# Performance work log

Hardware: AMD Instinct MI355X
Metric: run time of the kernel (lower is better)

## Reference

```python
import jax, jax.numpy as jnp
import numpy as np

N_NODES = 100000
N_EDGES = 1600000
F_IN = 512    # args.in_channels (original node feature dim)
F_GNN = 128   # GCNConv output / 'in_channels' ctor arg
HID = 64
Z_DIM = 64
N_GRAPHS = 512


def setup_inputs() -> dict:
    key = jax.random.key(0)
    ks = jax.random.split(key, 20)
    x = jax.random.normal(ks[0], (N_NODES, F_IN), dtype=jnp.float32)
    edge_index = jax.random.randint(ks[1], (2, N_EDGES), 0, N_NODES)
    batch = jnp.sort(jax.random.randint(ks[2], (N_NODES,), 0, N_GRAPHS))
    eps = jax.random.normal(ks[3], (N_GRAPHS, Z_DIM), dtype=jnp.float32)

    def lin(k, fi, fo):
        # xavier_uniform weight, zero bias
        lim = float(np.sqrt(6.0 / (fi + fo)))
        W = jax.random.uniform(k, (fi, fo), minval=-lim, maxval=lim, dtype=jnp.float32)
        return W, jnp.zeros((fo,), dtype=jnp.float32)

    Wg, bg = lin(ks[4], F_IN, F_GNN)
    We1, be1 = lin(ks[5], 2 * F_GNN, HID)
    We2, be2 = lin(ks[6], HID, HID)
    We3, be3 = lin(ks[7], HID, 2 * Z_DIM)
    Wd1, bd1 = lin(ks[8], Z_DIM, HID)
    Wd2, bd2 = lin(ks[9], HID, HID)
    Wd3, bd3 = lin(ks[10], HID, F_GNN)
    return {"x": x, "edge_index": edge_index, "batch": batch, "eps": eps,
            "Wg": Wg, "bg": bg,
            "We1": We1, "be1": be1, "We2": We2, "be2": be2, "We3": We3, "be3": be3,
            "Wd1": Wd1, "bd1": bd1, "Wd2": Wd2, "bd2": bd2, "Wd3": Wd3, "bd3": bd3}


def _gcn_conv(x, edge_index, Wg, bg):
    # PyG GCNConv: add self-loops, symmetric deg normalization, linear-then-aggregate
    n = x.shape[0]
    loops = jnp.arange(n)
    src = jnp.concatenate([edge_index[0], loops])
    dst = jnp.concatenate([edge_index[1], loops])
    deg = jax.ops.segment_sum(jnp.ones_like(dst, dtype=x.dtype), dst, num_segments=n)
    dinv = jnp.where(deg > 0, jax.lax.rsqrt(jnp.maximum(deg, 1.0)), 0.0)
    norm = dinv[src] * dinv[dst]              # [E+N]
    xw = x @ Wg                               # [N, F_GNN]
    msg = xw[src] * norm[:, None]             # gather + scale: [E+N, F_GNN]
    agg = jax.ops.segment_sum(msg, dst, num_segments=n)
    return agg + bg


def _forward(x, edge_index, batch, eps,
             Wg, bg, We1, be1, We2, be2, We3, be3,
             Wd1, bd1, Wd2, bd2, Wd3, bd3):
    n = x.shape[0]
    g = eps.shape[0]
    # single GNN layer (num_layers=1, JK='last'); dropout omitted (eval determinism)
    node_x = jax.nn.relu(_gcn_conv(x, edge_index, Wg, bg))  # [N, F_GNN]
    # global mean / max pool by graph id
    ones = jnp.ones((n,), dtype=node_x.dtype)
    cnt = jax.ops.segment_sum(ones, batch, num_segments=g)
    mean_p = jax.ops.segment_sum(node_x, batch, num_segments=g) / jnp.maximum(cnt, 1.0)[:, None]
    max_p = jax.ops.segment_max(node_x, batch, num_segments=g)
    graph_x = jnp.concatenate([mean_p, max_p], axis=1)      # [G, 2*F_GNN]
    # gaussian encoder MLP
    t = jax.nn.elu(graph_x @ We1 + be1)
    t = jnp.tanh(t @ We2 + be2)
    ml = t @ We3 + be3
    mu, logvar = jnp.split(ml, 2, axis=1)
    # reparameterise (note: module returns stddev in the 'logvar' slot)
    stddev = 1e-6 + jax.nn.softplus(logvar)
    z = mu + eps * stddev
    # bernoulli decoder MLP
    d = jnp.tanh(z @ Wd1 + bd1)
    d = jax.nn.elu(d @ Wd2 + bd2)
    y = jax.nn.sigmoid(d @ Wd3 + bd3)
    y = jnp.clip(y, 1e-8, 1.0 - 1e-8)
    return mu, stddev, y


def reference(x, edge_index, batch, eps,
              Wg, bg, We1, be1, We2, be2, We3, be3,
              Wd1, bd1, Wd2, bd2, Wd3, bd3):
    return _forward(x, edge_index, batch, eps,
                    Wg, bg, We1, be1, We2, be2, We3, be3,
                    Wd1, bd1, Wd2, bd2, Wd3, bd3)
```

## Files before the change

### kernel.cpp

```cpp
#include <hip/hip_runtime.h>
#include <hip/hip_bf16.h>
#include <math.h>

#define N_NODES 100000
#define N_EDGES 1600000
#define F_IN 512
#define F_GNN 128
#define HID 64
#define Z_DIM 64
#define N_GRAPHS 512
#define N_REGIONS 196
#define REGION_CAP 10240

typedef __attribute__((ext_vector_type(8))) short short8;
typedef __attribute__((ext_vector_type(4))) float f32x4;

__device__ __forceinline__ float eluf(float v) { return v > 0.f ? v : expm1f(v); }
__device__ __forceinline__ float softplusf(float v) {
  return fmaxf(v, 0.f) + log1pf(expf(-fabsf(v)));
}
__device__ __forceinline__ float sigmoidf(float v) { return 1.f / (1.f + expf(-v)); }

__device__ __forceinline__ unsigned short f2bf(float f) {
  unsigned int u = __float_as_uint(f);
  u = (u + 0x7fffu + ((u >> 16) & 1u)) >> 16;
  return (unsigned short)u;
}
__device__ __forceinline__ unsigned int f2bf2(float a, float b) {
  __hip_bfloat162 h = __float22bfloat162_rn(make_float2(a, b));
  unsigned int u;
  __builtin_memcpy(&u, &h, 4);
  return u;
}
__device__ __forceinline__ float bf_lo(unsigned int u) { return __uint_as_float(u << 16); }
__device__ __forceinline__ float bf_hi(unsigned int u) { return __uint_as_float(u & 0xffff0000u); }

__device__ __forceinline__ int lower_bound_i(const int* __restrict__ a, int n, int v) {
  int lo = 0, hi = n;
  while (lo < hi) {
    int mid = (lo + hi) >> 1;
    if (a[mid] < v) lo = mid + 1; else hi = mid;
  }
  return lo;
}

__global__ void k_wg(const float* __restrict__ Wg, unsigned short* __restrict__ WgT,
                     int* __restrict__ rcnt) {
  int i = blockIdx.x * 256 + threadIdx.x;
  if (blockIdx.x == 0) rcnt[threadIdx.x] = 0;
  int n = i >> 9, k = i & 511;
  WgT[i] = f2bf(Wg[k * F_GNN + n]);
}

__global__ __launch_bounds__(256) void k_rcount(const int* __restrict__ ei,
                                                int* __restrict__ rcnt) {
  __shared__ int lh[256];
  const int b = blockIdx.x, t = threadIdx.x;
  lh[t] = 0;
  __syncthreads();
#pragma unroll
  for (int j = 0; j < 8; j++) {
    int e = b * 2048 + t + 256 * j;
    if (e < N_EDGES) atomicAdd(&lh[ei[N_EDGES + e] >> 9], 1);
  }
  __syncthreads();
  if (t < N_REGIONS && lh[t] > 0) atomicAdd(&rcnt[t], lh[t]);
}

__global__ __launch_bounds__(256) void k_rscan(int* __restrict__ rcnt,
                                               int* __restrict__ rbase) {
  __shared__ int s[256];
  int t = threadIdx.x;
  s[t] = (t < N_REGIONS) ? rcnt[t] : 0;
  __syncthreads();
#pragma unroll
  for (int d = 1; d < 256; d <<= 1) {
    int v = (t >= d) ? s[t - d] : 0;
    __syncthreads();
    s[t] += v;
    __syncthreads();
  }
  int excl = (t > 0) ? s[t - 1] : 0;
  rbase[t] = excl;
  rcnt[t] = excl;
  if (t == 255) rbase[N_REGIONS] = s[255];
}

__global__ __launch_bounds__(256) void k_bucket(
    const int* __restrict__ ei, int* __restrict__ cursor_r,
    uint2* __restrict__ pairs) {
  __shared__ int lhist[256];
  __shared__ int lofs[256];
  __shared__ int lcur[256];
  __shared__ int gbase[256];
  __shared__ int sc[256];
  __shared__ uint2 lpairs[4096];

  const int b = blockIdx.x, t = threadIdx.x;
  const int e0 = b * 4096;
  const int n_b = min(4096, N_EDGES - e0);

  lhist[t] = 0;
  lcur[t] = 0;
  __syncthreads();

  int srcv[16], dstv[16];
#pragma unroll
  for (int j = 0; j < 16; j++) {
    int e = e0 + t + 256 * j;
    if (e < N_EDGES) {
      srcv[j] = ei[e];
      dstv[j] = ei[N_EDGES + e];
      atomicAdd(&lhist[dstv[j] >> 9], 1);
    } else {
      dstv[j] = -1;
    }
  }
  __syncthreads();

  sc[t] = lhist[t];
  __syncthreads();
#pragma unroll
  for (int d = 1; d < 256; d <<= 1) {
    int v = (t >= d) ? sc[t - d] : 0;
    __syncthreads();
    sc[t] += v;
    __syncthreads();
  }
  lofs[t] = (t > 0) ? sc[t - 1] : 0;
  if (t < N_REGIONS && lhist[t] > 0) gbase[t] = atomicAdd(&cursor_r[t], lhist[t]);
  __syncthreads();

#pragma unroll
  for (int j = 0; j < 16; j++) {
    if (dstv[j] >= 0) {
      int r = dstv[j] >> 9;
      int pos = lofs[r] + atomicAdd(&lcur[r], 1);
      lpairs[pos] = make_uint2((unsigned)srcv[j], (unsigned)dstv[j]);
    }
  }
  __syncthreads();

  for (int i = t; i < n_b; i += 256) {
    int lo = 0, hi = N_REGIONS;
    while (hi - lo > 1) {
      int mid = (lo + hi) >> 1;
      if (lofs[mid] <= i) lo = mid; else hi = mid;
    }
    pairs[gbase[lo] + (i - lofs[lo])] = lpairs[i];
  }
}

__global__ __launch_bounds__(256) void k_region(
    const uint2* __restrict__ pairs, const int* __restrict__ rbase,
    int* __restrict__ off, float* __restrict__ dinv, int* __restrict__ csr_src) {
  __shared__ int nh[512];
  __shared__ int sofs[512];
  __shared__ int sc[256];
  __shared__ int ncur[512];
  __shared__ int cbuf[REGION_CAP];

  const int r = blockIdx.x, t = threadIdx.x;
  const int base = rbase[r];
  const int cnt = rbase[r + 1] - base;

  nh[t] = 0;
  nh[t + 256] = 0;
  __syncthreads();

  for (int i = t; i < cnt; i += 256) {
    uint2 p = pairs[base + i];
    atomicAdd(&nh[p.y & 511], 1);
  }
  __syncthreads();

  int a0 = nh[2 * t], a1 = nh[2 * t + 1];
  sc[t] = a0 + a1;
  __syncthreads();
#pragma unroll
  for (int d = 1; d < 256; d <<= 1) {
    int v = (t >= d) ? sc[t - d] : 0;
    __syncthreads();
    sc[t] += v;
    __syncthreads();
  }
  int excl = (t > 0) ? sc[t - 1] : 0;
  sofs[2 * t] = excl;
  sofs[2 * t + 1] = excl + a0;

  const int node0 = r << 9;
  int n0 = node0 + 2 * t;
  if (n0 < N_NODES)     { off[n0] = base + excl;      dinv[n0] = rsqrtf(1.f + (float)a0); }
  if (n0 + 1 < N_NODES) { off[n0 + 1] = base + excl + a0; dinv[n0 + 1] = rsqrtf(1.f + (float)a1); }
  if (r == N_REGIONS - 1 && t == 0) off[N_NODES] = N_EDGES;

  ncur[t] = 0;
  ncur[t + 256] = 0;
  __syncthreads();

  for (int i = t; i < cnt; i += 256) {
    uint2 p = pairs[base + i];
    int d = (int)p.y & 511;
    int lpos = sofs[d] + atomicAdd(&ncur[d], 1);
    if (lpos < REGION_CAP) cbuf[lpos] = (int)p.x;
  }
  __syncthreads();
  for (int i = t; i < cnt; i += 256) csr_src[base + i] = cbuf[i];
}

__global__ __launch_bounds__(256) void k_gemm(
    const float* __restrict__ x, const unsigned short* __restrict__ WgT,
    const float* __restrict__ dinv, unsigned short* __restrict__ sxw) {
  __shared__ unsigned short As[128][32];
  __shared__ unsigned short Bs[128][32];

  const int t = threadIdx.x;
  const int lane15 = t & 15;
  const int quad = (t & 63) >> 4;
  const int wave = t >> 6;
  const int wm = (wave & 1) * 64;
  const int wn = (wave >> 1) * 64;
  const int row0 = blockIdx.x * 128;

  f32x4 acc[4][4];
#pragma unroll
  for (int mi = 0; mi < 4; mi++)
#pragma unroll
    for (int ni = 0; ni < 4; ni++) acc[mi][ni] = (f32x4){0.f, 0.f, 0.f, 0.f};

  float4 ga[4];
  uint4 gb[2];
  auto load_tile = [&](int k0) {
#pragma unroll
    for (int i = 0; i < 4; i++) {
      int f = t + 256 * i;
      int r = f >> 3, c4 = f & 7;
      int gr = row0 + r;
      if (gr >= N_NODES) gr = N_NODES - 1;
      ga[i] = *(const float4*)&x[(size_t)gr * F_IN + k0 + c4 * 4];
    }
#pragma unroll
    for (int i = 0; i < 2; i++) {
      int f = t + 256 * i;
      int r = f >> 2, c = f & 3;
      gb[i] = *(const uint4*)&WgT[r * F_IN + k0 + c * 8];
    }
  };

  load_tile(0);
#pragma unroll 1
  for (int kt = 0; kt < 16; kt++) {
    __syncthreads();
#pragma unroll
    for (int i = 0; i < 4; i++) {
      int f = t + 256 * i;
      int r = f >> 3, c4 = f & 7;
      unsigned int u0 = f2bf2(ga[i].x, ga[i].y);
      unsigned int u1 = f2bf2(ga[i].z, ga[i].w);
      *(uint2*)&As[r][c4 * 4] = make_uint2(u0, u1);
    }
#pragma unroll
    for (int i = 0; i < 2; i++) {
      int f = t + 256 * i;
      int r = f >> 2, c = f & 3;
      *(uint4*)&Bs[r][c * 8] = gb[i];
    }
    __syncthreads();
    if (kt < 15) load_tile((kt + 1) * 32);

    short8 afr[4], bfr[4];
#pragma unroll
    for (int mi = 0; mi < 4; mi++)
      afr[mi] = *(const short8*)&As[wm + mi * 16 + lane15][quad * 8];
#pragma unroll
    for (int ni = 0; ni < 4; ni++)
      bfr[ni] = *(const short8*)&Bs[wn + ni * 16 + lane15][quad * 8];
#pragma unroll
    for (int mi = 0; mi < 4; mi++)
#pragma unroll
      for (int ni = 0; ni < 4; ni++)
        acc[mi][ni] = __builtin_amdgcn_mfma_f32_16x16x32_bf16(
            bfr[ni], afr[mi], acc[mi][ni], 0, 0, 0);
  }

#pragma unroll
  for (int mi = 0; mi < 4; mi++) {
    int gm = row0 + wm + mi * 16 + lane15;
    if (gm < N_NODES) {
      float s = dinv[gm];
#pragma unroll
      for (int ni = 0; ni < 4; ni++) {
        int gn = wn + ni * 16 + quad * 4;
        unsigned int u0 = f2bf2(acc[mi][ni][0] * s, acc[mi][ni][1] * s);
        unsigned int u1 = f2bf2(acc[mi][ni][2] * s, acc[mi][ni][3] * s);
        *(uint2*)&sxw[(size_t)gm * F_GNN + gn] = make_uint2(u0, u1);
      }
    }
  }
}

__global__ __launch_bounds__(1024) void k_aggpool(
    const unsigned short* __restrict__ sxw, const int* __restrict__ off,
    const int* __restrict__ csr_src, const float* __restrict__ dinv,
    const float* __restrict__ bg, const int* __restrict__ batch,
    float* __restrict__ gx) {
  __shared__ float2 ssum[16][64];
  __shared__ float2 smax[16][64];
  __shared__ int sse[2];
  const int g = blockIdx.x;
  const int t = threadIdx.x;
  const int wv = t >> 6;
  const int lane = t & 63;

  if (t == 0) sse[0] = lower_bound_i(batch, N_NODES, g);
  if (t == 64) sse[1] = lower_bound_i(batch, N_NODES, g + 1);
  __syncthreads();
  const int start = sse[0], end = sse[1];

  const unsigned int* S = (const unsigned int*)sxw;
  float2 b = ((const float2*)bg)[lane];
  float2 ps = make_float2(0.f, 0.f);
  float2 pm = make_float2(0.f, 0.f);

  for (int node = start + wv; node < end; node += 16) {
    unsigned int u = S[(size_t)node * 64 + lane];
    float sx = bf_lo(u), sy = bf_hi(u);
    int e = off[node];
    int e1 = off[node + 1];
    for (; e + 7 < e1; e += 8) {
      int s0 = csr_src[e + 0], s1 = csr_src[e + 1];
      int s2 = csr_src[e + 2], s3 = csr_src[e + 3];
      int s4 = csr_src[e + 4], s5 = csr_src[e + 5];
      int s6 = csr_src[e + 6], s7 = csr_src[e + 7];
      unsigned int v0 = S[(size_t)s0 * 64 + lane];
      unsigned int v1 = S[(size_t)s1 * 64 + lane];
      unsigned int v2 = S[(size_t)s2 * 64 + lane];
      unsigned int v3 = S[(size_t)s3 * 64 + lane];
      unsigned int v4 = S[(size_t)s4 * 64 + lane];
      unsigned int v5 = S[(size_t)s5 * 64 + lane];
      unsigned int v6 = S[(size_t)s6 * 64 + lane];
      unsigned int v7 = S[(size_t)s7 * 64 + lane];
      sx += bf_lo(v0) + bf_lo(v1) + bf_lo(v2) + bf_lo(v3)
          + bf_lo(v4) + bf_lo(v5) + bf_lo(v6) + bf_lo(v7);
      sy += bf_hi(v0) + bf_hi(v1) + bf_hi(v2) + bf_hi(v3)
          + bf_hi(v4) + bf_hi(v5) + bf_hi(v6) + bf_hi(v7);
    }
    for (; e < e1; e++) {
      unsigned int v0 = S[(size_t)csr_src[e] * 64 + lane];
      sx += bf_lo(v0);
      sy += bf_hi(v0);
    }
    float di = dinv[node];
    float rx = fmaxf(fmaf(sx, di, b.x), 0.f);
    float ry = fmaxf(fmaf(sy, di, b.y), 0.f);
    ps.x += rx; ps.y += ry;
    pm.x = fmaxf(pm.x, rx); pm.y = fmaxf(pm.y, ry);
  }

  ssum[wv][lane] = ps;
  smax[wv][lane] = pm;
  __syncthreads();
  if (t < 64) {
    float2 s = ssum[0][t];
    float2 m = smax[0][t];
#pragma unroll
    for (int h = 1; h < 16; h++) {
      s.x += ssum[h][t].x; s.y += ssum[h][t].y;
      m.x = fmaxf(m.x, smax[h][t].x); m.y = fmaxf(m.y, smax[h][t].y);
    }
    float ic = 1.f / fmaxf((float)(end - start), 1.f);
    gx[g * 256 + 2 * t] = s.x * ic;
    gx[g * 256 + 2 * t + 1] = s.y * ic;
    gx[g * 256 + 128 + 2 * t] = m.x;
    gx[g * 256 + 129 + 2 * t] = m.y;
  }
}

__global__ __launch_bounds__(64) void k_mlp(
    const float* __restrict__ gx, const float* __restrict__ eps,
    const float* __restrict__ We1, const float* __restrict__ be1,
    const float* __restrict__ We2, const float* __restrict__ be2,
    const float* __restrict__ We3, const float* __restrict__ be3,
    const float* __restrict__ Wd1, const float* __restrict__ bd1,
    const float* __restrict__ Wd2, const float* __restrict__ bd2,
    const float* __restrict__ Wd3, const float* __restrict__ bd3,
    float* __restrict__ out) {
  __shared__ float row[256];
  __shared__ float t1[64], t2[64], zz[64], d1[64], d2[64];
  int g = blockIdx.x;
  int j = threadIdx.x;

#pragma unroll
  for (int i = 0; i < 4; i++) row[j + 64 * i] = gx[g * 256 + j + 64 * i];
  __syncthreads();

  float s = be1[j];
#pragma unroll 4
  for (int k = 0; k < 256; k++) s = fmaf(row[k], We1[k * 64 + j], s);
  t1[j] = eluf(s);
  __syncthreads();

  s = be2[j];
#pragma unroll 4
  for (int k = 0; k < 64; k++) s = fmaf(t1[k], We2[k * 64 + j], s);
  t2[j] = tanhf(s);
  __syncthreads();

  float m = be3[j], lv = be3[64 + j];
#pragma unroll 4
  for (int k = 0; k < 64; k++) {
    float tv = t2[k];
    m = fmaf(tv, We3[k * 128 + j], m);
    lv = fmaf(tv, We3[k * 128 + 64 + j], lv);
  }
  float sd = 1e-6f + softplusf(lv);
  float z = fmaf(eps[g * 64 + j], sd, m);
  out[g * 64 + j] = m;
  out[32768 + g * 64 + j] = sd;
  zz[j] = z;
  __syncthreads();

  s = bd1[j];
#pragma unroll 4
  for (int k = 0; k < 64; k++) s = fmaf(zz[k], Wd1[k * 64 + j], s);
  d1[j] = tanhf(s);
  __syncthreads();

  s = bd2[j];
#pragma unroll 4
  for (int k = 0; k < 64; k++) s = fmaf(d1[k], Wd2[k * 64 + j], s);
  d2[j] = eluf(s);
  __syncthreads();

  float y0 = bd3[j], y1 = bd3[64 + j];
#pragma unroll 4
  for (int k = 0; k < 64; k++) {
    float dv = d2[k];
    y0 = fmaf(dv, Wd3[k * 128 + j], y0);
    y1 = fmaf(dv, Wd3[k * 128 + 64 + j], y1);
  }
  y0 = fminf(fmaxf(sigmoidf(y0), 1e-8f), 1.f - 1e-8f);
  y1 = fminf(fmaxf(sigmoidf(y1), 1e-8f), 1.f - 1e-8f);
  out[65536 + g * 128 + j] = y0;
  out[65536 + g * 128 + 64 + j] = y1;
}

extern "C" void kernel_launch(void* const* d_in, const int* in_sizes, int n_in,
                              void* d_out, int out_size, void* d_ws, size_t ws_size,
                              hipStream_t stream) {
  const float* x     = (const float*)d_in[0];
  const int*   ei    = (const int*)d_in[1];
  const int*   batch = (const int*)d_in[2];
  const float* eps   = (const float*)d_in[3];
  const float* Wg    = (const float*)d_in[4];
  const float* bg    = (const float*)d_in[5];
  const float* We1   = (const float*)d_in[6];
  const float* be1   = (const float*)d_in[7];
  const float* We2   = (const float*)d_in[8];
  const float* be2   = (const float*)d_in[9];
  const float* We3   = (const float*)d_in[10];
  const float* be3   = (const float*)d_in[11];
  const float* Wd1   = (const float*)d_in[12];
  const float* bd1   = (const float*)d_in[13];
  const float* Wd2   = (const float*)d_in[14];
  const float* bd2   = (const float*)d_in[15];
  const float* Wd3   = (const float*)d_in[16];
  const float* bd3   = (const float*)d_in[17];
  float* out = (float*)d_out;

  int*            rbase    = (int*)d_ws;
  int*            cursor_r = rbase + 256;
  int*            off      = cursor_r + 256;
  float*          dinv     = (float*)(off + 102656);
  int*            csr_src  = (int*)(dinv + 102400);
  uint2*          pairs    = (uint2*)(csr_src + 1600128);
  unsigned short* WgT      = (unsigned short*)(pairs + 1600000);
  unsigned short* sxw      = WgT + 65536;
  float*          gx       = (float*)(sxw + 12800000);

  k_wg<<<(F_IN * F_GNN) / 256, 256, 0, stream>>>(Wg, WgT, cursor_r);
  k_rcount<<<(N_EDGES + 2047) / 2048, 256, 0, stream>>>(ei, cursor_r);
  k_rscan<<<1, 256, 0, stream>>>(cursor_r, rbase);
  k_bucket<<<(N_EDGES + 4095) / 4096, 256, 0, stream>>>(ei, cursor_r, pairs);
  k_region<<<N_REGIONS, 256, 0, stream>>>(pairs, rbase, off, dinv, csr_src);
  k_gemm<<<(N_NODES + 127) / 128, 256, 0, stream>>>(x, WgT, dinv, sxw);
  k_aggpool<<<N_GRAPHS, 1024, 0, stream>>>(sxw, off, csr_src, dinv, bg, batch, gx);
  k_mlp<<<N_GRAPHS, 64, 0, stream>>>(gx, eps, We1, be1, We2, be2, We3, be3,
                                     Wd1, bd1, Wd2, bd2, Wd3, bd3, out);
}
```

Measured before the change: 559.4 us.

## Replace CSR build with region-bucketed shared-memory atomic aggregation and atomic pooling

```diff
diff --git a/kernel.cpp b/kernel.cpp
--- a/kernel.cpp
+++ b/kernel.cpp
@@ -10,7 +10,7 @@
 #define Z_DIM 64
 #define N_GRAPHS 512
 #define N_REGIONS 196
-#define REGION_CAP 10240
+#define QTR 128
 
 typedef __attribute__((ext_vector_type(8))) short short8;
 typedef __attribute__((ext_vector_type(4))) float f32x4;
@@ -35,36 +35,46 @@
 __device__ __forceinline__ float bf_lo(unsigned int u) { return __uint_as_float(u << 16); }
 __device__ __forceinline__ float bf_hi(unsigned int u) { return __uint_as_float(u & 0xffff0000u); }
 
-__device__ __forceinline__ int lower_bound_i(const int* __restrict__ a, int n, int v) {
-  int lo = 0, hi = n;
-  while (lo < hi) {
-    int mid = (lo + hi) >> 1;
-    if (a[mid] < v) lo = mid + 1; else hi = mid;
-  }
-  return lo;
-}
-
-__global__ void k_wg(const float* __restrict__ Wg, unsigned short* __restrict__ WgT,
-                     int* __restrict__ rcnt) {
+__global__ __launch_bounds__(256) void k_init(
+    const float* __restrict__ Wg, unsigned short* __restrict__ WgT,
+    int* __restrict__ hist, float* __restrict__ gx, float* __restrict__ gcnt) {
   int i = blockIdx.x * 256 + threadIdx.x;
-  if (blockIdx.x == 0) rcnt[threadIdx.x] = 0;
-  int n = i >> 9, k = i & 511;
-  WgT[i] = f2bf(Wg[k * F_GNN + n]);
-}
-
-__global__ __launch_bounds__(256) void k_rcount(const int* __restrict__ ei,
-                                                int* __restrict__ rcnt) {
-  __shared__ int lh[256];
-  const int b = blockIdx.x, t = threadIdx.x;
-  lh[t] = 0;
-  __syncthreads();
-#pragma unroll
-  for (int j = 0; j < 8; j++) {
-    int e = b * 2048 + t + 256 * j;
-    if (e < N_EDGES) atomicAdd(&lh[ei[N_EDGES + e] >> 9], 1);
-  }
-  __syncthreads();
-  if (t < N_REGIONS && lh[t] > 0) atomicAdd(&rcnt[t], lh[t]);
+  if (i < 65536) {
+    int n = i >> 9, k = i & 511;
+    WgT[i] = f2bf(Wg[k * F_GNN + n]);
+  }
+  if (i < 100352) hist[i] = 0;
+  gx[i] = 0.f;
+  if (i < 512) gcnt[i] = 0.f;
+}
+
+__global__ __launch_bounds__(256) void k_hist(const int* __restrict__ ei,
+                                              int* __restrict__ hist) {
+  int b = blockIdx.x, t = threadIdx.x;
+#pragma unroll
+  for (int j = 0; j < 4; j++) {
+    int e = b * 1024 + t + 256 * j;
+    if (e < N_EDGES) atomicAdd(&hist[ei[N_EDGES + e]], 1);
+  }
+}
+
+__global__ __launch_bounds__(256) void k_rsum(const int* __restrict__ hist,
+                                              float* __restrict__ dinv,
+                                              int* __restrict__ rcnt) {
+  __shared__ int s[256];
+  int r = blockIdx.x, t = threadIdx.x;
+  int n0 = (r << 9) + 2 * t;
+  int a0 = hist[n0], a1 = hist[n0 + 1];
+  if (n0 < N_NODES)     dinv[n0]     = rsqrtf(1.f + (float)a0);
+  if (n0 + 1 < N_NODES) dinv[n0 + 1] = rsqrtf(1.f + (float)a1);
+  s[t] = a0 + a1;
+  __syncthreads();
+#pragma unroll
+  for (int d = 128; d > 0; d >>= 1) {
+    if (t < d) s[t] += s[t + d];
+    __syncthreads();
+  }
+  if (t == 0) rcnt[r] = s[0];
 }
 
 __global__ __launch_bounds__(256) void k_rscan(int* __restrict__ rcnt,
@@ -88,13 +98,13 @@
 
 __global__ __launch_bounds__(256) void k_bucket(
     const int* __restrict__ ei, int* __restrict__ cursor_r,
-    uint2* __restrict__ pairs) {
+    unsigned int* __restrict__ pairs) {
   __shared__ int lhist[256];
   __shared__ int lofs[256];
   __shared__ int lcur[256];
   __shared__ int gbase[256];
   __shared__ int sc[256];
-  __shared__ uint2 lpairs[4096];
+  __shared__ unsigned int lpairs[4096];
 
   const int b = blockIdx.x, t = threadIdx.x;
   const int e0 = b * 4096;
@@ -136,7 +146,7 @@
     if (dstv[j] >= 0) {
       int r = dstv[j] >> 9;
       int pos = lofs[r] + atomicAdd(&lcur[r], 1);
-      lpairs[pos] = make_uint2((unsigned)srcv[j], (unsigned)dstv[j]);
+      lpairs[pos] = (unsigned)srcv[j] | ((unsigned)(dstv[j] & 511) << 17);
     }
   }
   __syncthreads();
@@ -149,63 +159,6 @@
     }
     pairs[gbase[lo] + (i - lofs[lo])] = lpairs[i];
   }
-}
-
-__global__ __launch_bounds__(256) void k_region(
-    const uint2* __restrict__ pairs, const int* __restrict__ rbase,
-    int* __restrict__ off, float* __restrict__ dinv, int* __restrict__ csr_src) {
-  __shared__ int nh[512];
-  __shared__ int sofs[512];
-  __shared__ int sc[256];
-  __shared__ int ncur[512];
-  __shared__ int cbuf[REGION_CAP];
-
-  const int r = blockIdx.x, t = threadIdx.x;
-  const int base = rbase[r];
-  const int cnt = rbase[r + 1] - base;
-
-  nh[t] = 0;
-  nh[t + 256] = 0;
-  __syncthreads();
-
-  for (int i = t; i < cnt; i += 256) {
-    uint2 p = pairs[base + i];
-    atomicAdd(&nh[p.y & 511], 1);
-  }
-  __syncthreads();
-
-  int a0 = nh[2 * t], a1 = nh[2 * t + 1];
-  sc[t] = a0 + a1;
-  __syncthreads();
-#pragma unroll
-  for (int d = 1; d < 256; d <<= 1) {
-    int v = (t >= d) ? sc[t - d] : 0;
-    __syncthreads();
-    sc[t] += v;
-    __syncthreads();
-  }
-  int excl = (t > 0) ? sc[t - 1] : 0;
-  sofs[2 * t] = excl;
-  sofs[2 * t + 1] = excl + a0;
-
-  const int node0 = r << 9;
-  int n0 = node0 + 2 * t;
-  if (n0 < N_NODES)     { off[n0] = base + excl;      dinv[n0] = rsqrtf(1.f + (float)a0); }
-  if (n0 + 1 < N_NODES) { off[n0 + 1] = base + excl + a0; dinv[n0 + 1] = rsqrtf(1.f + (float)a1); }
-  if (r == N_REGIONS - 1 && t == 0) off[N_NODES] = N_EDGES;
-
-  ncur[t] = 0;
-  ncur[t + 256] = 0;
-  __syncthreads();
-
-  for (int i = t; i < cnt; i += 256) {
-    uint2 p = pairs[base + i];
-    int d = (int)p.y & 511;
-    int lpos = sofs[d] + atomicAdd(&ncur[d], 1);
-    if (lpos < REGION_CAP) cbuf[lpos] = (int)p.x;
-  }
-  __syncthreads();
-  for (int i = t; i < cnt; i += 256) csr_src[base + i] = cbuf[i];
 }
 
 __global__ __launch_bounds__(256) void k_gemm(
@@ -299,85 +252,112 @@
   }
 }
 
-__global__ __launch_bounds__(1024) void k_aggpool(
-    const unsigned short* __restrict__ sxw, const int* __restrict__ off,
-    const int* __restrict__ csr_src, const float* __restrict__ dinv,
+__global__ __launch_bounds__(512) void k_regagg(
+    const unsigned int* __restrict__ pairs, const int* __restrict__ rbase,
+    const unsigned short* __restrict__ sxw, const float* __restrict__ dinv,
     const float* __restrict__ bg, const int* __restrict__ batch,
-    float* __restrict__ gx) {
-  __shared__ float2 ssum[16][64];
-  __shared__ float2 smax[16][64];
-  __shared__ int sse[2];
-  const int g = blockIdx.x;
+    float* __restrict__ gx, float* __restrict__ gcnt) {
+  __shared__ float acc[QTR][F_GNN];
+
+  const int r = blockIdx.x >> 2;
+  const int q = blockIdx.x & 3;
   const int t = threadIdx.x;
-  const int wv = t >> 6;
-  const int lane = t & 63;
-
-  if (t == 0) sse[0] = lower_bound_i(batch, N_NODES, g);
-  if (t == 64) sse[1] = lower_bound_i(batch, N_NODES, g + 1);
-  __syncthreads();
-  const int start = sse[0], end = sse[1];
-
+  const int w = t >> 6, lane = t & 63;
+
+  float4* az = (float4*)acc;
+#pragma unroll
+  for (int i = 0; i < QTR * F_GNN / 4 / 512; i++)
+    az[t + 512 * i] = make_float4(0.f, 0.f, 0.f, 0.f);
+  __syncthreads();
+
+  const int base = rbase[r];
+  const int cnt = rbase[r + 1] - base;
   const unsigned int* S = (const unsigned int*)sxw;
+
+  for (int i0 = w * 8; i0 < cnt; i0 += 64) {
+    unsigned int pk[8], v[8];
+    int dl[8];
+    bool act[8];
+#pragma unroll
+    for (int j = 0; j < 8; j++) {
+      int e = i0 + j;
+      pk[j] = (e < cnt) ? pairs[base + e] : 0xFFFFFFFFu;
+    }
+#pragma unroll
+    for (int j = 0; j < 8; j++) {
+      dl[j] = (int)(pk[j] >> 17);
+      act[j] = (pk[j] != 0xFFFFFFFFu) && ((dl[j] >> 7) == q);
+      if (act[j]) v[j] = S[(size_t)(pk[j] & 0x1FFFFu) * 64 + lane];
+    }
+#pragma unroll
+    for (int j = 0; j < 8; j++) {
+      if (act[j]) {
+        int n = dl[j] & 127;
+        atomicAdd(&acc[n][2 * lane],     bf_lo(v[j]));
+        atomicAdd(&acc[n][2 * lane + 1], bf_hi(v[j]));
+      }
+    }
+  }
+  __syncthreads();
+
+  const int node0 = (r << 9) + (q << 7);
   float2 b = ((const float2*)bg)[lane];
-  float2 ps = make_float2(0.f, 0.f);
-  float2 pm = make_float2(0.f, 0.f);
-
-  for (int node = start + wv; node < end; node += 16) {
-    unsigned int u = S[(size_t)node * 64 + lane];
-    float sx = bf_lo(u), sy = bf_hi(u);
-    int e = off[node];
-    int e1 = off[node + 1];
-    for (; e + 7 < e1; e += 8) {
-      int s0 = csr_src[e + 0], s1 = csr_src[e + 1];
-      int s2 = csr_src[e + 2], s3 = csr_src[e + 3];
-      int s4 = csr_src[e + 4], s5 = csr_src[e + 5];
-      int s6 = csr_src[e + 6], s7 = csr_src[e + 7];
-      unsigned int v0 = S[(size_t)s0 * 64 + lane];
-      unsigned int v1 = S[(size_t)s1 * 64 + lane];
-      unsigned int v2 = S[(size_t)s2 * 64 + lane];
-      unsigned int v3 = S[(size_t)s3 * 64 + lane];
-      unsigned int v4 = S[(size_t)s4 * 64 + lane];
-      unsigned int v5 = S[(size_t)s5 * 64 + lane];
-      unsigned int v6 = S[(size_t)s6 * 64 + lane];
-      unsigned int v7 = S[(size_t)s7 * 64 + lane];
-      sx += bf_lo(v0) + bf_lo(v1) + bf_lo(v2) + bf_lo(v3)
-          + bf_lo(v4) + bf_lo(v5) + bf_lo(v6) + bf_lo(v7);
-      sy += bf_hi(v0) + bf_hi(v1) + bf_hi(v2) + bf_hi(v3)
-          + bf_hi(v4) + bf_hi(v5) + bf_hi(v6) + bf_hi(v7);
-    }
-    for (; e < e1; e++) {
-      unsigned int v0 = S[(size_t)csr_src[e] * 64 + lane];
-      sx += bf_lo(v0);
-      sy += bf_hi(v0);
-    }
-    float di = dinv[node];
-    float rx = fmaxf(fmaf(sx, di, b.x), 0.f);
-    float ry = fmaxf(fmaf(sy, di, b.y), 0.f);
-    ps.x += rx; ps.y += ry;
-    pm.x = fmaxf(pm.x, rx); pm.y = fmaxf(pm.y, ry);
-  }
-
-  ssum[wv][lane] = ps;
-  smax[wv][lane] = pm;
-  __syncthreads();
-  if (t < 64) {
-    float2 s = ssum[0][t];
-    float2 m = smax[0][t];
-#pragma unroll
-    for (int h = 1; h < 16; h++) {
-      s.x += ssum[h][t].x; s.y += ssum[h][t].y;
-      m.x = fmaxf(m.x, smax[h][t].x); m.y = fmaxf(m.y, smax[h][t].y);
-    }
-    float ic = 1.f / fmaxf((float)(end - start), 1.f);
-    gx[g * 256 + 2 * t] = s.x * ic;
-    gx[g * 256 + 2 * t + 1] = s.y * ic;
-    gx[g * 256 + 128 + 2 * t] = m.x;
-    gx[g * 256 + 129 + 2 * t] = m.y;
+  int curg = -1;
+  float psx = 0.f, psy = 0.f, pmx = 0.f, pmy = 0.f, pc = 0.f;
+
+  for (int k = 0; k < 16; k += 4) {
+    int nn[4], gg[4];
+    unsigned int sv[4];
+    float dv[4];
+    bool na[4];
+#pragma unroll
+    for (int j = 0; j < 4; j++) {
+      nn[j] = w + 8 * (k + j);
+      int node = node0 + nn[j];
+      na[j] = node < N_NODES;
+      if (na[j]) {
+        sv[j] = S[(size_t)node * 64 + lane];
+        gg[j] = batch[node];
+        dv[j] = dinv[node];
+      }
+    }
+#pragma unroll
+    for (int j = 0; j < 4; j++) {
+      if (!na[j]) continue;
+      float ax = acc[nn[j]][2 * lane]     + bf_lo(sv[j]);
+      float ay = acc[nn[j]][2 * lane + 1] + bf_hi(sv[j]);
+      float rx = fmaxf(fmaf(ax, dv[j], b.x), 0.f);
+      float ry = fmaxf(fmaf(ay, dv[j], b.y), 0.f);
+      if (gg[j] != curg) {
+        if (curg >= 0) {
+          atomicAdd(&gx[curg * 256 + 2 * lane],     psx);
+          atomicAdd(&gx[curg * 256 + 2 * lane + 1], psy);
+          atomicMax((unsigned int*)&gx[curg * 256 + 128 + 2 * lane],
+                    __float_as_uint(pmx));
+          atomicMax((unsigned int*)&gx[curg * 256 + 129 + 2 * lane],
+                    __float_as_uint(pmy));
+          if (lane == 0) atomicAdd(&gcnt[curg], pc);
+        }
+        curg = gg[j];
+        psx = psy = pmx = pmy = pc = 0.f;
+      }
+      psx += rx; psy += ry;
+      pmx = fmaxf(pmx, rx); pmy = fmaxf(pmy, ry);
+      pc += 1.f;
+    }
+  }
+  if (curg >= 0) {
+    atomicAdd(&gx[curg * 256 + 2 * lane],     psx);
+    atomicAdd(&gx[curg * 256 + 2 * lane + 1], psy);
+    atomicMax((unsigned int*)&gx[curg * 256 + 128 + 2 * lane], __float_as_uint(pmx));
+    atomicMax((unsigned int*)&gx[curg * 256 + 129 + 2 * lane], __float_as_uint(pmy));
+    if (lane == 0) atomicAdd(&gcnt[curg], pc);
   }
 }
 
 __global__ __launch_bounds__(64) void k_mlp(
-    const float* __restrict__ gx, const float* __restrict__ eps,
+    const float* __restrict__ gx, const float* __restrict__ gcnt,
+    const float* __restrict__ eps,
     const float* __restrict__ We1, const float* __restrict__ be1,
     const float* __restrict__ We2, const float* __restrict__ be2,
     const float* __restrict__ We3, const float* __restrict__ be3,
@@ -390,8 +370,13 @@
   int g = blockIdx.x;
   int j = threadIdx.x;
 
-#pragma unroll
-  for (int i = 0; i < 4; i++) row[j + 64 * i] = gx[g * 256 + j + 64 * i];
+  float ic = 1.f / fmaxf(gcnt[g], 1.f);
+#pragma unroll
+  for (int i = 0; i < 4; i++) {
+    float v = gx[g * 256 + j + 64 * i];
+    if (i < 2) v *= ic;
+    row[j + 64 * i] = v;
+  }
   __syncthreads();
 
   float s = be1[j];
@@ -468,23 +453,24 @@
   const float* bd3   = (const float*)d_in[17];
   float* out = (float*)d_out;
 
-  int*            rbase    = (int*)d_ws;
-  int*            cursor_r = rbase + 256;
-  int*            off      = cursor_r + 256;
-  float*          dinv     = (float*)(off + 102656);
-  int*            csr_src  = (int*)(dinv + 102400);
-  uint2*          pairs    = (uint2*)(csr_src + 1600128);
-  unsigned short* WgT      = (unsigned short*)(pairs + 1600000);
-  unsigned short* sxw      = WgT + 65536;
-  float*          gx       = (float*)(sxw + 12800000);
-
-  k_wg<<<(F_IN * F_GNN) / 256, 256, 0, stream>>>(Wg, WgT, cursor_r);
-  k_rcount<<<(N_EDGES + 2047) / 2048, 256, 0, stream>>>(ei, cursor_r);
-  k_rscan<<<1, 256, 0, stream>>>(cursor_r, rbase);
-  k_bucket<<<(N_EDGES + 4095) / 4096, 256, 0, stream>>>(ei, cursor_r, pairs);
-  k_region<<<N_REGIONS, 256, 0, stream>>>(pairs, rbase, off, dinv, csr_src);
+  int*            rbase = (int*)d_ws;
+  int*            rcnt  = rbase + 256;
+  int*            hist  = rcnt + 256;
+  float*          dinv  = (float*)(hist + 100352);
+  unsigned int*   pairs = (unsigned int*)(dinv + 100352);
+  unsigned short* WgT   = (unsigned short*)(pairs + 1600000);
+  unsigned short* sxw   = WgT + 65536;
+  float*          gx    = (float*)(sxw + 12800000);
+  float*          gcnt  = gx + 131072;
+
+  k_init<<<512, 256, 0, stream>>>(Wg, WgT, hist, gx, gcnt);
+  k_hist<<<(N_EDGES + 1023) / 1024, 256, 0, stream>>>(ei, hist);
+  k_rsum<<<N_REGIONS, 256, 0, stream>>>(hist, dinv, rcnt);
+  k_rscan<<<1, 256, 0, stream>>>(rcnt, rbase);
+  k_bucket<<<(N_EDGES + 4095) / 4096, 256, 0, stream>>>(ei, rcnt, pairs);
   k_gemm<<<(N_NODES + 127) / 128, 256, 0, stream>>>(x, WgT, dinv, sxw);
-  k_aggpool<<<N_GRAPHS, 1024, 0, stream>>>(sxw, off, csr_src, dinv, bg, batch, gx);
-  k_mlp<<<N_GRAPHS, 64, 0, stream>>>(gx, eps, We1, be1, We2, be2, We3, be3,
+  k_regagg<<<N_REGIONS * 4, 512, 0, stream>>>(pairs, rbase, sxw, dinv, bg, batch,
+                                              gx, gcnt);
+  k_mlp<<<N_GRAPHS, 64, 0, stream>>>(gx, gcnt, eps, We1, be1, We2, be2, We3, be3,
                                      Wd1, bd1, Wd2, bd2, Wd3, bd3, out);
 }
```

After: 1.845 ms. +229.8%, slower.

## Replace two-level region bucketing CSR build with global atomic histogram scatter

Applied to the files above, without the earlier changes.

```diff
diff --git a/kernel.cpp b/kernel.cpp
--- a/kernel.cpp
+++ b/kernel.cpp
@@ -10,7 +10,6 @@
 #define Z_DIM 64
 #define N_GRAPHS 512
 #define N_REGIONS 196
-#define REGION_CAP 10240
 
 typedef __attribute__((ext_vector_type(8))) short short8;
 typedef __attribute__((ext_vector_type(4))) float f32x4;
@@ -44,168 +43,94 @@
   return lo;
 }
 
-__global__ void k_wg(const float* __restrict__ Wg, unsigned short* __restrict__ WgT,
-                     int* __restrict__ rcnt) {
+__global__ __launch_bounds__(256) void k_init(
+    const float* __restrict__ Wg, unsigned short* __restrict__ WgT,
+    int* __restrict__ hist) {
   int i = blockIdx.x * 256 + threadIdx.x;
-  if (blockIdx.x == 0) rcnt[threadIdx.x] = 0;
-  int n = i >> 9, k = i & 511;
-  WgT[i] = f2bf(Wg[k * F_GNN + n]);
-}
-
-__global__ __launch_bounds__(256) void k_rcount(const int* __restrict__ ei,
-                                                int* __restrict__ rcnt) {
-  __shared__ int lh[256];
-  const int b = blockIdx.x, t = threadIdx.x;
-  lh[t] = 0;
-  __syncthreads();
+  if (i < 65536) {
+    int n = i >> 9, k = i & 511;
+    WgT[i] = f2bf(Wg[k * F_GNN + n]);
+  }
+  hist[i] = 0;
+}
+
+__global__ __launch_bounds__(256) void k_hist(const int* __restrict__ ei,
+                                              int* __restrict__ hist) {
+  int b = blockIdx.x, t = threadIdx.x;
+#pragma unroll
+  for (int j = 0; j < 4; j++) {
+    int e = b * 1024 + t + 256 * j;
+    if (e < N_EDGES) atomicAdd(&hist[ei[N_EDGES + e]], 1);
+  }
+}
+
+__global__ __launch_bounds__(256) void k_scan1(const int* __restrict__ hist,
+                                               int* __restrict__ off,
+                                               int* __restrict__ bsum) {
+  __shared__ int s[256];
+  int b = blockIdx.x, t = threadIdx.x;
+  int i0 = b * 512 + 2 * t;
+  int a0 = (i0 < N_NODES) ? hist[i0] : 0;
+  int a1 = (i0 + 1 < N_NODES) ? hist[i0 + 1] : 0;
+  s[t] = a0 + a1;
+  __syncthreads();
+#pragma unroll
+  for (int d = 1; d < 256; d <<= 1) {
+    int v = (t >= d) ? s[t - d] : 0;
+    __syncthreads();
+    s[t] += v;
+    __syncthreads();
+  }
+  int excl = (t > 0) ? s[t - 1] : 0;
+  if (i0 < N_NODES) off[i0] = excl;
+  if (i0 + 1 < N_NODES) off[i0 + 1] = excl + a0;
+  if (t == 255) bsum[b] = s[255];
+}
+
+__global__ __launch_bounds__(256) void k_scan2(const int* __restrict__ bsum,
+                                               int* __restrict__ boff) {
+  __shared__ int s[256];
+  int t = threadIdx.x;
+  s[t] = (t < N_REGIONS) ? bsum[t] : 0;
+  __syncthreads();
+#pragma unroll
+  for (int d = 1; d < 256; d <<= 1) {
+    int v = (t >= d) ? s[t - d] : 0;
+    __syncthreads();
+    s[t] += v;
+    __syncthreads();
+  }
+  boff[t] = (t > 0) ? s[t - 1] : 0;
+}
+
+__global__ __launch_bounds__(256) void k_scan3(int* __restrict__ off,
+                                               const int* __restrict__ boff,
+                                               const int* __restrict__ hist,
+                                               float* __restrict__ dinv,
+                                               int* __restrict__ cursor) {
+  int i = blockIdx.x * 256 + threadIdx.x;
+  if (i < N_NODES) {
+    int o = off[i] + boff[i >> 9];
+    off[i] = o;
+    cursor[i] = o;
+    dinv[i] = rsqrtf(1.0f + (float)hist[i]);
+  }
+  if (i == 0) off[N_NODES] = N_EDGES;
+}
+
+__global__ __launch_bounds__(256) void k_scatter(const int* __restrict__ ei,
+                                                 int* __restrict__ cursor,
+                                                 int* __restrict__ csr_src) {
+  int b = blockIdx.x, t = threadIdx.x;
 #pragma unroll
   for (int j = 0; j < 8; j++) {
     int e = b * 2048 + t + 256 * j;
-    if (e < N_EDGES) atomicAdd(&lh[ei[N_EDGES + e] >> 9], 1);
-  }
-  __syncthreads();
-  if (t < N_REGIONS && lh[t] > 0) atomicAdd(&rcnt[t], lh[t]);
-}
-
-__global__ __launch_bounds__(256) void k_rscan(int* __restrict__ rcnt,
-                                               int* __restrict__ rbase) {
-  __shared__ int s[256];
-  int t = threadIdx.x;
-  s[t] = (t < N_REGIONS) ? rcnt[t] : 0;
-  __syncthreads();
-#pragma unroll
-  for (int d = 1; d < 256; d <<= 1) {
-    int v = (t >= d) ? s[t - d] : 0;
-    __syncthreads();
-    s[t] += v;
-    __syncthreads();
-  }
-  int excl = (t > 0) ? s[t - 1] : 0;
-  rbase[t] = excl;
-  rcnt[t] = excl;
-  if (t == 255) rbase[N_REGIONS] = s[255];
-}
-
-__global__ __launch_bounds__(256) void k_bucket(
-    const int* __restrict__ ei, int* __restrict__ cursor_r,
-    uint2* __restrict__ pairs) {
-  __shared__ int lhist[256];
-  __shared__ int lofs[256];
-  __shared__ int lcur[256];
-  __shared__ int gbase[256];
-  __shared__ int sc[256];
-  __shared__ uint2 lpairs[4096];
-
-  const int b = blockIdx.x, t = threadIdx.x;
-  const int e0 = b * 4096;
-  const int n_b = min(4096, N_EDGES - e0);
-
-  lhist[t] = 0;
-  lcur[t] = 0;
-  __syncthreads();
-
-  int srcv[16], dstv[16];
-#pragma unroll
-  for (int j = 0; j < 16; j++) {
-    int e = e0 + t + 256 * j;
     if (e < N_EDGES) {
-      srcv[j] = ei[e];
-      dstv[j] = ei[N_EDGES + e];
-      atomicAdd(&lhist[dstv[j] >> 9], 1);
-    } else {
-      dstv[j] = -1;
-    }
-  }
-  __syncthreads();
-
-  sc[t] = lhist[t];
-  __syncthreads();
-#pragma unroll
-  for (int d = 1; d < 256; d <<= 1) {
-    int v = (t >= d) ? sc[t - d] : 0;
-    __syncthreads();
-    sc[t] += v;
-    __syncthreads();
-  }
-  lofs[t] = (t > 0) ? sc[t - 1] : 0;
-  if (t < N_REGIONS && lhist[t] > 0) gbase[t] = atomicAdd(&cursor_r[t], lhist[t]);
-  __syncthreads();
-
-#pragma unroll
-  for (int j = 0; j < 16; j++) {
-    if (dstv[j] >= 0) {
-      int r = dstv[j] >> 9;
-      int pos = lofs[r] + atomicAdd(&lcur[r], 1);
-      lpairs[pos] = make_uint2((unsigned)srcv[j], (unsigned)dstv[j]);
-    }
-  }
-  __syncthreads();
-
-  for (int i = t; i < n_b; i += 256) {
-    int lo = 0, hi = N_REGIONS;
-    while (hi - lo > 1) {
-      int mid = (lo + hi) >> 1;
-      if (lofs[mid] <= i) lo = mid; else hi = mid;
-    }
-    pairs[gbase[lo] + (i - lofs[lo])] = lpairs[i];
-  }
-}
-
-__global__ __launch_bounds__(256) void k_region(
-    const uint2* __restrict__ pairs, const int* __restrict__ rbase,
-    int* __restrict__ off, float* __restrict__ dinv, int* __restrict__ csr_src) {
-  __shared__ int nh[512];
-  __shared__ int sofs[512];
-  __shared__ int sc[256];
-  __shared__ int ncur[512];
-  __shared__ int cbuf[REGION_CAP];
-
-  const int r = blockIdx.x, t = threadIdx.x;
-  const int base = rbase[r];
-  const int cnt = rbase[r + 1] - base;
-
-  nh[t] = 0;
-  nh[t + 256] = 0;
-  __syncthreads();
-
-  for (int i = t; i < cnt; i += 256) {
-    uint2 p = pairs[base + i];
-    atomicAdd(&nh[p.y & 511], 1);
-  }
-  __syncthreads();
-
-  int a0 = nh[2 * t], a1 = nh[2 * t + 1];
-  sc[t] = a0 + a1;
-  __syncthreads();
-#pragma unroll
-  for (int d = 1; d < 256; d <<= 1) {
-    int v = (t >= d) ? sc[t - d] : 0;
-    __syncthreads();
-    sc[t] += v;
-    __syncthreads();
-  }
-  int excl = (t > 0) ? sc[t - 1] : 0;
-  sofs[2 * t] = excl;
-  sofs[2 * t + 1] = excl + a0;
-
-  const int node0 = r << 9;
-  int n0 = node0 + 2 * t;
-  if (n0 < N_NODES)     { off[n0] = base + excl;      dinv[n0] = rsqrtf(1.f + (float)a0); }
-  if (n0 + 1 < N_NODES) { off[n0 + 1] = base + excl + a0; dinv[n0 + 1] = rsqrtf(1.f + (float)a1); }
-  if (r == N_REGIONS - 1 && t == 0) off[N_NODES] = N_EDGES;
-
-  ncur[t] = 0;
-  ncur[t + 256] = 0;
-  __syncthreads();
-
-  for (int i = t; i < cnt; i += 256) {
-    uint2 p = pairs[base + i];
-    int d = (int)p.y & 511;
-    int lpos = sofs[d] + atomicAdd(&ncur[d], 1);
-    if (lpos < REGION_CAP) cbuf[lpos] = (int)p.x;
-  }
-  __syncthreads();
-  for (int i = t; i < cnt; i += 256) csr_src[base + i] = cbuf[i];
+      int dst = ei[N_EDGES + e];
+      int pos = atomicAdd(&cursor[dst], 1);
+      csr_src[pos] = ei[e];
+    }
+  }
 }
 
 __global__ __launch_bounds__(256) void k_gemm(
@@ -468,21 +393,23 @@
   const float* bd3   = (const float*)d_in[17];
   float* out = (float*)d_out;
 
-  int*            rbase    = (int*)d_ws;
-  int*            cursor_r = rbase + 256;
-  int*            off      = cursor_r + 256;
-  float*          dinv     = (float*)(off + 102656);
-  int*            csr_src  = (int*)(dinv + 102400);
-  uint2*          pairs    = (uint2*)(csr_src + 1600128);
-  unsigned short* WgT      = (unsigned short*)(pairs + 1600000);
-  unsigned short* sxw      = WgT + 65536;
-  float*          gx       = (float*)(sxw + 12800000);
-
-  k_wg<<<(F_IN * F_GNN) / 256, 256, 0, stream>>>(Wg, WgT, cursor_r);
-  k_rcount<<<(N_EDGES + 2047) / 2048, 256, 0, stream>>>(ei, cursor_r);
-  k_rscan<<<1, 256, 0, stream>>>(cursor_r, rbase);
-  k_bucket<<<(N_EDGES + 4095) / 4096, 256, 0, stream>>>(ei, cursor_r, pairs);
-  k_region<<<N_REGIONS, 256, 0, stream>>>(pairs, rbase, off, dinv, csr_src);
+  int*            hist    = (int*)d_ws;
+  int*            off     = hist + 100352;
+  float*          dinv    = (float*)(off + 100608);
+  int*            cursor  = (int*)(dinv + 100352);
+  int*            bsum    = cursor + 100352;
+  int*            boff    = bsum + 256;
+  int*            csr_src = boff + 256;
+  unsigned short* WgT     = (unsigned short*)(csr_src + 1600000);
+  unsigned short* sxw     = WgT + 65536;
+  float*          gx      = (float*)(sxw + 12800000);
+
+  k_init<<<392, 256, 0, stream>>>(Wg, WgT, hist);
+  k_hist<<<(N_EDGES + 1023) / 1024, 256, 0, stream>>>(ei, hist);
+  k_scan1<<<N_REGIONS, 256, 0, stream>>>(hist, off, bsum);
+  k_scan2<<<1, 256, 0, stream>>>(bsum, boff);
+  k_scan3<<<392, 256, 0, stream>>>(off, boff, hist, dinv, cursor);
+  k_scatter<<<(N_EDGES + 2047) / 2048, 256, 0, stream>>>(ei, cursor, csr_src);
   k_gemm<<<(N_NODES + 127) / 128, 256, 0, stream>>>(x, WgT, dinv, sxw);
   k_aggpool<<<N_GRAPHS, 1024, 0, stream>>>(sxw, off, csr_src, dinv, bg, batch, gx);
   k_mlp<<<N_GRAPHS, 64, 0, stream>>>(gx, eps, We1, be1, We2, be2, We3, be3,
```

Result: slower. 704.5 us (+25.9%).
